# Performance work log

Measured on AMD Instinct MI355X. Metric: run time of the kernel, lower is better.

## Reference

```python
import jax, jax.numpy as jnp
import numpy as np

# config constants (init_kwargs)
S, C, N, DK, DA = 4, 1024, 131072, 128, 2048
M_TOP, K_MAX, B, T = 32, 64, 64, 1.0
EPS = 1e-8


def setup_inputs() -> dict:
    key = jax.random.key(0)
    k0, k1, k2, k3 = jax.random.split(key, 4)
    return {
        "z": jax.random.normal(k0, (B, DA), jnp.float32),
        "pool_keys": jax.random.normal(k1, (S, N, DK), jnp.float32),
        "W_Q": jax.random.normal(k2, (S, DK, DA), jnp.float32) * DA ** -0.5,
        "aspect_weights": jnp.zeros((S,), jnp.float32),
        "tau": jnp.zeros((), jnp.float32),
        "centroids": jax.random.normal(k3, (S, C, DK), jnp.float32) * DK ** -0.5,
        "lambda_val": jnp.ones((), jnp.float32),
        "is_warmup": 0,
    }


def _l2norm(x):
    return x / (jnp.linalg.norm(x, axis=-1, keepdims=True) + EPS)


def reference(z, pool_keys, W_Q, aspect_weights, tau, centroids, lambda_val, is_warmup):
    Bb = z.shape[0]
    # aspect queries: [B, S, d_k]
    queries = jnp.einsum('ska,ba->bsk', W_Q, z)
    q_norm = _l2norm(queries)
    w = jax.nn.softmax(aspect_weights, axis=0)  # [S]

    # --- IVF stage 1: centroid search ---
    c_norm = _l2norm(centroids)                     # [S, C, d_k]
    c_sim = jnp.einsum('bsk,sck->bsc', q_norm, c_norm)
    c_score = jnp.einsum('s,bsc->bc', w, c_sim)      # [B, C]
    m_eff = min(M_TOP, C)
    _, top_clusters = jax.lax.top_k(c_score, m_eff)  # [B, m]

    # --- IVF stage 2: refine within selected clusters ---
    n_per_c = N // C
    cand_idx = (top_clusters[:, :, None] * n_per_c
                + jnp.arange(n_per_c)[None, None, :]).reshape(Bb, m_eff * n_per_c)  # [B, M]
    # gather candidate keys: [S, B, M, d_k] -> [B, S, M, d_k]
    keys_refine = jnp.take(pool_keys, cand_idx, axis=1).transpose(1, 0, 2, 3)
    k_norm = _l2norm(keys_refine)
    sim_ref = jnp.einsum('bsk,bsnk->bsn', q_norm, k_norm)
    s_i = jnp.einsum('s,bsn->bn', w, sim_ref)        # [B, M]

    # --- redundant full dense pass for soft_full ---
    p_norm_full = _l2norm(pool_keys)                 # [S, N, d_k]
    sim_all = jnp.einsum('bsk,snk->bsn', q_norm, p_norm_full)
    s_i_full = jnp.einsum('s,bsn->bn', w, sim_all)   # [B, N]
    soft_full = jax.nn.softmax(s_i_full / T, axis=-1)

    if is_warmup:
        scores, local_idx = jax.lax.top_k(s_i, K_MAX)
        global_idx = jnp.take_along_axis(cand_idx, local_idx, axis=1)
        alphas = jax.nn.softmax(scores / T, axis=-1)
    else:
        g = jax.nn.sigmoid(lambda_val * (s_i - tau))
        raw = g * jnp.exp(s_i / T)
        raw = raw / (raw.sum(axis=-1, keepdims=True) + EPS)
        top_raw, local_idx = jax.lax.top_k(raw, K_MAX)
        global_idx = jnp.take_along_axis(cand_idx, local_idx, axis=1)
        alphas = top_raw / (top_raw.sum(axis=-1, keepdims=True) + EPS)
    return alphas, global_idx, soft_full
```

## Files before the change

### kernel.cpp

```cpp
#include <hip/hip_runtime.h>
#include <math.h>

#define S_N   4
#define C_N   1024
#define N_N   131072
#define DK_N  128
#define DA_N  2048
#define MTOP  32
#define KMAX  64
#define B_N   64
#define NPC   128
#define MCAND 4096
#define KTOT  512
#define EPSF  1e-8f

__global__ void k_init(float* sums) { sums[threadIdx.x] = 0.0f; }

__global__ __launch_bounds__(256) void k_queries(const float* __restrict__ z,
                                                 const float* __restrict__ wqm,
                                                 const float* __restrict__ aw,
                                                 float* __restrict__ qw) {
    __shared__ __align__(16) float zl[DA_N];
    __shared__ float ql[DK_N];
    __shared__ float red[2];
    const int t = threadIdx.x;
    const int s = blockIdx.x >> 6;
    const int b = blockIdx.x & 63;
    const float4* zr = (const float4*)(z + (size_t)b * DA_N);
    float4* zl4 = (float4*)zl;
    for (int i = t; i < DA_N / 4; i += 256) zl4[i] = zr[i];
    __syncthreads();
    const int wave = t >> 6, lane = t & 63;
    for (int kw = 0; kw < 32; ++kw) {
        int k = wave * 32 + kw;
        const float* wr = wqm + ((size_t)(s * DK_N + k)) * DA_N;
        float acc = 0.f;
        #pragma unroll
        for (int i = 0; i < 32; ++i) acc += wr[i * 64 + lane] * zl[i * 64 + lane];
        for (int m = 32; m >= 1; m >>= 1) acc += __shfl_xor(acc, m, 64);
        if (lane == 0) ql[k] = acc;
    }
    __syncthreads();
    if (t < 128) {
        float v = ql[t];
        float p = v * v;
        for (int m = 32; m >= 1; m >>= 1) p += __shfl_xor(p, m, 64);
        if ((t & 63) == 0) red[t >> 6] = p;
    }
    __syncthreads();
    if (t < 128) {
        float ss = red[0] + red[1];
        float inv = 1.0f / (sqrtf(ss) + EPSF);
        float a0 = aw[0], a1 = aw[1], a2 = aw[2], a3 = aw[3];
        float mx = fmaxf(fmaxf(a0, a1), fmaxf(a2, a3));
        float e0 = expf(a0 - mx), e1 = expf(a1 - mx), e2 = expf(a2 - mx), e3 = expf(a3 - mx);
        float wsum = e0 + e1 + e2 + e3;
        float wv = (s == 0 ? e0 : s == 1 ? e1 : s == 2 ? e2 : e3) / wsum;
        qw[(size_t)b * KTOT + s * DK_N + t] = wv * inv * ql[t];
    }
}

__global__ __launch_bounds__(256) void k_cnorm(const float* __restrict__ cent,
                                               float* __restrict__ cn) {
    const int t = threadIdx.x;
    const int wave = t >> 6, lane = t & 63;
    const int row = blockIdx.x * 4 + wave;
    const float2* cr = (const float2*)(cent + (size_t)row * DK_N);
    float2 v = cr[lane];
    float p = v.x * v.x + v.y * v.y;
    for (int m = 32; m >= 1; m >>= 1) p += __shfl_xor(p, m, 64);
    float inv = 1.0f / (sqrtf(p) + EPSF);
    float2* o = (float2*)(cn + (size_t)row * DK_N);
    o[lane] = make_float2(v.x * inv, v.y * inv);
}

__global__ __launch_bounds__(256) void k_cscore(const float* __restrict__ qw,
                                                const float* __restrict__ cn,
                                                double* __restrict__ cs) {
    __shared__ __align__(16) float qwl[KTOT];
    const int t = threadIdx.x;
    const int b = blockIdx.x >> 2;
    const int cq = blockIdx.x & 3;
    qwl[t] = qw[(size_t)b * KTOT + t];
    qwl[t + 256] = qw[(size_t)b * KTOT + t + 256];
    __syncthreads();
    const int c = cq * 256 + t;
    double acc = 0.0;
    #pragma unroll
    for (int s = 0; s < 4; ++s) {
        const float* qs = qwl + s * DK_N;
        const float4* cp = (const float4*)(cn + ((size_t)(s * C_N + c)) * DK_N);
        #pragma unroll 8
        for (int k4 = 0; k4 < 32; ++k4) {
            float4 f = cp[k4];
            acc += (double)qs[k4 * 4 + 0] * f.x + (double)qs[k4 * 4 + 1] * f.y
                 + (double)qs[k4 * 4 + 2] * f.z + (double)qs[k4 * 4 + 3] * f.w;
        }
    }
    cs[(size_t)b * C_N + c] = acc;
}

__global__ __launch_bounds__(256) void k_top32(const double* __restrict__ cs,
                                               int* __restrict__ topc,
                                               int* __restrict__ invm) {
    __shared__ double val[C_N];
    __shared__ double wvs[4];
    __shared__ int wis[4];
    const int t = threadIdx.x;
    const int b = blockIdx.x;
    #pragma unroll
    for (int r = 0; r < 4; ++r) {
        val[r * 256 + t] = cs[(size_t)b * C_N + r * 256 + t];
        invm[b * C_N + r * 256 + t] = -1;
    }
    __syncthreads();
    for (int it = 0; it < MTOP; ++it) {
        double bv = -1e300; int bi = -1;
        #pragma unroll
        for (int r = 0; r < 4; ++r) {
            int cc = r * 256 + t;
            double v = val[cc];
            if (v > bv || (v == bv && (unsigned)cc < (unsigned)bi)) { bv = v; bi = cc; }
        }
        for (int m = 32; m >= 1; m >>= 1) {
            double ov = __shfl_xor(bv, m, 64);
            int oi = __shfl_xor(bi, m, 64);
            if (ov > bv || (ov == bv && (unsigned)oi < (unsigned)bi)) { bv = ov; bi = oi; }
        }
        if ((t & 63) == 0) { wvs[t >> 6] = bv; wis[t >> 6] = bi; }
        __syncthreads();
        if (t == 0) {
            double cbv = wvs[0]; int cbi = wis[0];
            for (int w = 1; w < 4; ++w)
                if (wvs[w] > cbv || (wvs[w] == cbv && (unsigned)wis[w] < (unsigned)cbi)) { cbv = wvs[w]; cbi = wis[w]; }
            topc[b * MTOP + it] = cbi;
            invm[b * C_N + cbi] = it;
            val[cbi] = -1e300;
        }
        __syncthreads();
    }
}

__global__ __launch_bounds__(256, 4) void k_dense(const float* __restrict__ keys,
                                                  const float* __restrict__ qw,
                                                  const int* __restrict__ invm,
                                                  double* __restrict__ si,
                                                  float* __restrict__ out_soft,
                                                  float* __restrict__ sums) {
    __shared__ __align__(16) float keyl[32 * 196];
    __shared__ __align__(16) float qwl[32 * 68];
    __shared__ float invn[128];
    __shared__ int hb[64], hj[64];
    __shared__ int hcnt;
    const int t = threadIdx.x;
    const int cl = blockIdx.x;
    const int n0 = cl * NPC;
    if (t == 0) hcnt = 0;
    __syncthreads();
    if (t < 64) {
        int j = invm[t * C_N + cl];
        if (j >= 0) { int p = atomicAdd(&hcnt, 1); hb[p] = t; hj[p] = j; }
    }
    const int nq = t & 15, bq = t >> 4;
    float acc[4][8];
    #pragma unroll
    for (int i = 0; i < 4; ++i)
        #pragma unroll
        for (int j = 0; j < 8; ++j) acc[i][j] = 0.f;

    for (int c = 0; c < 16; ++c) {
        const int s = c >> 2;
        const int koff = (c & 3) * 32;
        if ((c & 3) == 0) {
            __syncthreads();
            int row = t >> 1, half = t & 1;
            const float4* kp4 = (const float4*)(keys + ((size_t)(s * N_N + n0 + row)) * DK_N + half * 64);
            float ssq = 0.f;
            #pragma unroll
            for (int i = 0; i < 16; ++i) {
                float4 f = kp4[i];
                ssq += f.x * f.x + f.y * f.y + f.z * f.z + f.w * f.w;
            }
            ssq += __shfl_xor(ssq, 1, 64);
            if (half == 0) invn[row] = 1.0f / (sqrtf(ssq) + EPSF);
            __syncthreads();
        }
        #pragma unroll
        for (int rep = 0; rep < 4; ++rep) {
            int idx = rep * 256 + t;
            int kk4 = idx & 7;
            int n = idx >> 3;
            const float4 v = *(const float4*)(keys + ((size_t)(s * N_N + n0 + n)) * DK_N + koff + kk4 * 4);
            float sc = invn[n];
            int noffn = n + ((n >> 3) << 2);
            float vv[4] = {v.x * sc, v.y * sc, v.z * sc, v.w * sc};
            #pragma unroll
            for (int jj = 0; jj < 4; ++jj) {
                int j2 = (kk4 + jj) & 3;
                keyl[(kk4 * 4 + j2) * 196 + noffn] = vv[j2];
            }
        }
        #pragma unroll
        for (int rep = 0; rep < 2; ++rep) {
            int idx = rep * 256 + t;
            int kk4 = idx & 7;
            int b = idx >> 3;
            const float4 v = *(const float4*)(qw + (size_t)b * KTOT + c * 32 + kk4 * 4);
            float vv[4] = {v.x, v.y, v.z, v.w};
            #pragma unroll
            for (int jj = 0; jj < 4; ++jj) {
                int j2 = (kk4 + jj) & 3;
                qwl[(kk4 * 4 + j2) * 68 + b] = vv[j2];
            }
        }
        __syncthreads();
        #pragma unroll 4
        for (int k = 0; k < 32; ++k) {
            const float4 qv = *(const float4*)&qwl[k * 68 + bq * 4];
            const float4 ka = *(const float4*)&keyl[k * 196 + nq * 12];
            const float4 kb = *(const float4*)&keyl[k * 196 + nq * 12 + 4];
            const float qr[4] = {qv.x, qv.y, qv.z, qv.w};
            const float kr[8] = {ka.x, ka.y, ka.z, ka.w, kb.x, kb.y, kb.z, kb.w};
            #pragma unroll
            for (int i = 0; i < 4; ++i)
                #pragma unroll
                for (int j = 0; j < 8; ++j)
                    acc[i][j] += qr[i] * kr[j];
        }
        const int nh = hcnt;
        for (int h = 0; h < nh; ++h) {
            const int b = hb[h], j = hj[h];
            const int n = t >> 1, half = t & 1;
            const int noffn = n + ((n >> 3) << 2);
            double a = 0.0;
            #pragma unroll
            for (int kk2 = 0; kk2 < 16; ++kk2) {
                int kk = half * 16 + kk2;
                a += (double)qwl[kk * 68 + b] * (double)keyl[kk * 196 + noffn];
            }
            a += __shfl_xor(a, 1, 64);
            if (half == 0) {
                double* sp = si + (size_t)b * MCAND + j * NPC + n;
                if (c == 0) *sp = a;
                else *sp += a;
            }
        }
        __syncthreads();
    }
    #pragma unroll
    for (int i = 0; i < 4; ++i) {
        int b = bq * 4 + i;
        float e[8]; float se = 0.f;
        #pragma unroll
        for (int j = 0; j < 8; ++j) { e[j] = expf(acc[i][j]); se += e[j]; }
        float4* op = (float4*)(out_soft + (size_t)b * N_N + n0 + nq * 8);
        op[0] = make_float4(e[0], e[1], e[2], e[3]);
        op[1] = make_float4(e[4], e[5], e[6], e[7]);
        #pragma unroll
        for (int m = 8; m >= 1; m >>= 1) se += __shfl_xor(se, m, 16);
        if ((t & 15) == 0) atomicAdd(&sums[b], se);
    }
}

__global__ __launch_bounds__(256) void k_top64(const double* __restrict__ si,
                                               const int* __restrict__ topc,
                                               const float* __restrict__ taup,
                                               const float* __restrict__ lamp,
                                               const int* __restrict__ warmp,
                                               float* __restrict__ out_alpha,
                                               float* __restrict__ out_idx) {
    __shared__ double key64[MCAND];
    __shared__ float aux[MCAND];
    __shared__ double rs[4];
    __shared__ double wvs[4];
    __shared__ int wis[4];
    __shared__ int sel[KMAX];
    const int t = threadIdx.x;
    const int b = blockIdx.x;
    const int warm = *warmp;
    const float lamf = *lamp, tauf = *taup;
    double loc = 0.0;
    for (int r = 0; r < 16; ++r) {
        int j = r * 256 + t;
        double sd = si[(size_t)b * MCAND + j];
        float sf = (float)sd;
        if (warm) {
            key64[j] = sd;
            aux[j] = sf;
        } else {
            float g = 1.0f / (1.0f + expf(-lamf * (sf - tauf)));
            float raw = g * expf(sf);
            aux[j] = raw;
            loc += (double)raw;
            double x = (double)lamf * (sd - (double)tauf);
            key64[j] = sd - log1p(exp(-x));
        }
    }
    for (int m = 32; m >= 1; m >>= 1) loc += __shfl_xor(loc, m, 64);
    if ((t & 63) == 0) rs[t >> 6] = loc;
    __syncthreads();
    const float S_all = (float)(rs[0] + rs[1] + rs[2] + rs[3]);
    for (int it = 0; it < KMAX; ++it) {
        double bv = -1e300; int bi = -1;
        for (int r = 0; r < 16; ++r) {
            int j = r * 256 + t;
            double v = key64[j];
            if (v > bv || (v == bv && (unsigned)j < (unsigned)bi)) { bv = v; bi = j; }
        }
        for (int m = 32; m >= 1; m >>= 1) {
            double ov = __shfl_xor(bv, m, 64);
            int oi = __shfl_xor(bi, m, 64);
            if (ov > bv || (ov == bv && (unsigned)oi < (unsigned)bi)) { bv = ov; bi = oi; }
        }
        if ((t & 63) == 0) { wvs[t >> 6] = bv; wis[t >> 6] = bi; }
        __syncthreads();
        if (t == 0) {
            double cbv = wvs[0]; int cbi = wis[0];
            for (int w = 1; w < 4; ++w)
                if (wvs[w] > cbv || (wvs[w] == cbv && (unsigned)wis[w] < (unsigned)cbi)) { cbv = wvs[w]; cbi = wis[w]; }
            sel[it] = cbi;
            key64[cbi] = -1e300;
        }
        __syncthreads();
    }
    if (t < KMAX) {
        int j = sel[t];
        float numer;
        if (warm) numer = expf(aux[j]);
        else numer = aux[j] / (S_all + EPSF);
        float tot = numer;
        for (int m = 32; m >= 1; m >>= 1) tot += __shfl_xor(tot, m, 64);
        float denom = warm ? tot : (tot + EPSF);
        float alpha = numer / denom;
        out_alpha[b * KMAX + t] = alpha;
        int cl2 = topc[b * MTOP + (j >> 7)];
        out_idx[b * KMAX + t] = (float)(cl2 * NPC + (j & 127));
    }
}

__global__ void k_norm(float* __restrict__ out_soft, const float* __restrict__ sums) {
    const int b = blockIdx.x >> 7;
    const int p = (blockIdx.x & 127) * 256 + threadIdx.x;
    const float inv = 1.0f / sums[b];
    float4* p4 = (float4*)(out_soft + (size_t)b * N_N) + p;
    float4 v = *p4;
    v.x *= inv; v.y *= inv; v.z *= inv; v.w *= inv;
    *p4 = v;
}

extern "C" void kernel_launch(void* const* d_in, const int* in_sizes, int n_in,
                              void* d_out, int out_size, void* d_ws, size_t ws_size,
                              hipStream_t stream) {
    const float* z    = (const float*)d_in[0];
    const float* keys = (const float*)d_in[1];
    const float* wqm  = (const float*)d_in[2];
    const float* aw   = (const float*)d_in[3];
    const float* tau  = (const float*)d_in[4];
    const float* cent = (const float*)d_in[5];
    const float* lam  = (const float*)d_in[6];
    const int*   warm = (const int*)d_in[7];
    float* out = (float*)d_out;
    float* out_alpha = out;
    float* out_idx   = out + B_N * KMAX;
    float* out_soft  = out + 2 * B_N * KMAX;
    char* ws = (char*)d_ws;
    float*  qw   = (float*)(ws + 0);
    float*  cn   = (float*)(ws + 131072);
    double* cs   = (double*)(ws + 2228224);
    int*    topc = (int*)(ws + 2752512);
    int*    invm = (int*)(ws + 2760704);
    double* si   = (double*)(ws + 3022848);
    float*  sums = (float*)(ws + 5120000);

    hipLaunchKernelGGL(k_init,    dim3(1),    dim3(64),  0, stream, sums);
    hipLaunchKernelGGL(k_queries, dim3(256),  dim3(256), 0, stream, z, wqm, aw, qw);
    hipLaunchKernelGGL(k_cnorm,   dim3(1024), dim3(256), 0, stream, cent, cn);
    hipLaunchKernelGGL(k_cscore,  dim3(256),  dim3(256), 0, stream, qw, cn, cs);
    hipLaunchKernelGGL(k_top32,   dim3(64),   dim3(256), 0, stream, cs, topc, invm);
    hipLaunchKernelGGL(k_dense,   dim3(1024), dim3(256), 0, stream, keys, qw, invm, si, out_soft, sums);
    hipLaunchKernelGGL(k_top64,   dim3(64),   dim3(256), 0, stream, si, topc, tau, lam, warm, out_alpha, out_idx);
    hipLaunchKernelGGL(k_norm,    dim3(8192), dim3(256), 0, stream, out_soft, sums);
}
```

Before: 758.4 us.

## Use bf16 MFMA for dense similarity, parallelize top-64 and centroid scoring

Result: faster. 688.0 us (-9.3%).

```diff
diff --git a/kernel.cpp b/kernel.cpp
--- a/kernel.cpp
+++ b/kernel.cpp
@@ -13,6 +13,15 @@
 #define MCAND 4096
 #define KTOT  512
 #define EPSF  1e-8f
+#define KPAD  40
+
+typedef short s8v __attribute__((ext_vector_type(8)));
+typedef float f4v __attribute__((ext_vector_type(4)));
+
+__device__ __forceinline__ unsigned short f2bf(float x) {
+    unsigned u = __float_as_uint(x);
+    return (unsigned short)((u + 0x7FFFu + ((u >> 16) & 1u)) >> 16);
+}
 
 __global__ void k_init(float* sums) { sums[threadIdx.x] = 0.0f; }
 
@@ -78,26 +87,27 @@
                                                 const float* __restrict__ cn,
                                                 double* __restrict__ cs) {
     __shared__ __align__(16) float qwl[KTOT];
-    const int t = threadIdx.x;
-    const int b = blockIdx.x >> 2;
-    const int cq = blockIdx.x & 3;
+    __shared__ double part[4][64];
+    const int t = threadIdx.x;
+    const int b = blockIdx.x >> 4;
+    const int cq = blockIdx.x & 15;
     qwl[t] = qw[(size_t)b * KTOT + t];
     qwl[t + 256] = qw[(size_t)b * KTOT + t + 256];
     __syncthreads();
-    const int c = cq * 256 + t;
+    const int cl = t & 63, s = t >> 6;
+    const int c = cq * 64 + cl;
+    const float* qs = qwl + s * DK_N;
+    const float4* cp = (const float4*)(cn + ((size_t)(s * C_N + c)) * DK_N);
     double acc = 0.0;
-    #pragma unroll
-    for (int s = 0; s < 4; ++s) {
-        const float* qs = qwl + s * DK_N;
-        const float4* cp = (const float4*)(cn + ((size_t)(s * C_N + c)) * DK_N);
-        #pragma unroll 8
-        for (int k4 = 0; k4 < 32; ++k4) {
-            float4 f = cp[k4];
-            acc += (double)qs[k4 * 4 + 0] * f.x + (double)qs[k4 * 4 + 1] * f.y
-                 + (double)qs[k4 * 4 + 2] * f.z + (double)qs[k4 * 4 + 3] * f.w;
-        }
-    }
-    cs[(size_t)b * C_N + c] = acc;
+    #pragma unroll 8
+    for (int k4 = 0; k4 < 32; ++k4) {
+        float4 f = cp[k4];
+        acc += (double)qs[k4 * 4 + 0] * f.x + (double)qs[k4 * 4 + 1] * f.y
+             + (double)qs[k4 * 4 + 2] * f.z + (double)qs[k4 * 4 + 3] * f.w;
+    }
+    part[s][cl] = acc;
+    __syncthreads();
+    if (t < 64) cs[(size_t)b * C_N + cq * 64 + t] = part[0][t] + part[1][t] + part[2][t] + part[3][t];
 }
 
 __global__ __launch_bounds__(256) void k_top32(const double* __restrict__ cs,
@@ -147,26 +157,29 @@
                                                   double* __restrict__ si,
                                                   float* __restrict__ out_soft,
                                                   float* __restrict__ sums) {
-    __shared__ __align__(16) float keyl[32 * 196];
-    __shared__ __align__(16) float qwl[32 * 68];
+    __shared__ __align__(16) unsigned short keyl[128 * KPAD];
+    __shared__ __align__(16) unsigned short qbl[64 * KPAD];
+    __shared__ float qf32l[32 * 68];
     __shared__ float invn[128];
+    __shared__ double hacc[8 * 128];
     __shared__ int hb[64], hj[64];
     __shared__ int hcnt;
     const int t = threadIdx.x;
     const int cl = blockIdx.x;
     const int n0 = cl * NPC;
+    const int lane = t & 63, w = t >> 6;
+    const int quad = lane >> 4, col = lane & 15;
     if (t == 0) hcnt = 0;
+    for (int i = t; i < 1024; i += 256) hacc[i] = 0.0;
     __syncthreads();
     if (t < 64) {
         int j = invm[t * C_N + cl];
         if (j >= 0) { int p = atomicAdd(&hcnt, 1); hb[p] = t; hj[p] = j; }
     }
-    const int nq = t & 15, bq = t >> 4;
-    float acc[4][8];
+
+    f4v acc[8];
     #pragma unroll
-    for (int i = 0; i < 4; ++i)
-        #pragma unroll
-        for (int j = 0; j < 8; ++j) acc[i][j] = 0.f;
+    for (int T = 0; T < 8; ++T) acc[T] = (f4v){0.f, 0.f, 0.f, 0.f};
 
     for (int c = 0; c < 16; ++c) {
         const int s = c >> 2;
@@ -192,13 +205,9 @@
             int n = idx >> 3;
             const float4 v = *(const float4*)(keys + ((size_t)(s * N_N + n0 + n)) * DK_N + koff + kk4 * 4);
             float sc = invn[n];
-            int noffn = n + ((n >> 3) << 2);
-            float vv[4] = {v.x * sc, v.y * sc, v.z * sc, v.w * sc};
-            #pragma unroll
-            for (int jj = 0; jj < 4; ++jj) {
-                int j2 = (kk4 + jj) & 3;
-                keyl[(kk4 * 4 + j2) * 196 + noffn] = vv[j2];
-            }
+            unsigned w0 = (unsigned)f2bf(v.x * sc) | ((unsigned)f2bf(v.y * sc) << 16);
+            unsigned w1 = (unsigned)f2bf(v.z * sc) | ((unsigned)f2bf(v.w * sc) << 16);
+            *(uint2*)&keyl[n * KPAD + kk4 * 4] = make_uint2(w0, w1);
         }
         #pragma unroll
         for (int rep = 0; rep < 2; ++rep) {
@@ -206,59 +215,68 @@
             int kk4 = idx & 7;
             int b = idx >> 3;
             const float4 v = *(const float4*)(qw + (size_t)b * KTOT + c * 32 + kk4 * 4);
-            float vv[4] = {v.x, v.y, v.z, v.w};
-            #pragma unroll
-            for (int jj = 0; jj < 4; ++jj) {
-                int j2 = (kk4 + jj) & 3;
-                qwl[(kk4 * 4 + j2) * 68 + b] = vv[j2];
-            }
+            unsigned w0 = (unsigned)f2bf(v.x) | ((unsigned)f2bf(v.y) << 16);
+            unsigned w1 = (unsigned)f2bf(v.z) | ((unsigned)f2bf(v.w) << 16);
+            *(uint2*)&qbl[b * KPAD + kk4 * 4] = make_uint2(w0, w1);
+            qf32l[(kk4 * 4 + 0) * 68 + b] = v.x;
+            qf32l[(kk4 * 4 + 1) * 68 + b] = v.y;
+            qf32l[(kk4 * 4 + 2) * 68 + b] = v.z;
+            qf32l[(kk4 * 4 + 3) * 68 + b] = v.w;
         }
         __syncthreads();
-        #pragma unroll 4
-        for (int k = 0; k < 32; ++k) {
-            const float4 qv = *(const float4*)&qwl[k * 68 + bq * 4];
-            const float4 ka = *(const float4*)&keyl[k * 196 + nq * 12];
-            const float4 kb = *(const float4*)&keyl[k * 196 + nq * 12 + 4];
-            const float qr[4] = {qv.x, qv.y, qv.z, qv.w};
-            const float kr[8] = {ka.x, ka.y, ka.z, ka.w, kb.x, kb.y, kb.z, kb.w};
-            #pragma unroll
-            for (int i = 0; i < 4; ++i)
-                #pragma unroll
-                for (int j = 0; j < 8; ++j)
-                    acc[i][j] += qr[i] * kr[j];
+        const s8v a_frag = *(const s8v*)&qbl[(w * 16 + col) * KPAD + quad * 8];
+        #pragma unroll
+        for (int T = 0; T < 8; ++T) {
+            const s8v b_frag = *(const s8v*)&keyl[(T * 16 + col) * KPAD + quad * 8];
+            acc[T] = __builtin_amdgcn_mfma_f32_16x16x32_bf16(a_frag, b_frag, acc[T], 0, 0, 0);
         }
         const int nh = hcnt;
         for (int h = 0; h < nh; ++h) {
             const int b = hb[h], j = hj[h];
             const int n = t >> 1, half = t & 1;
-            const int noffn = n + ((n >> 3) << 2);
+            const float4* kp = (const float4*)(keys + ((size_t)(s * N_N + n0 + n)) * DK_N + koff + half * 16);
             double a = 0.0;
             #pragma unroll
-            for (int kk2 = 0; kk2 < 16; ++kk2) {
-                int kk = half * 16 + kk2;
-                a += (double)qwl[kk * 68 + b] * (double)keyl[kk * 196 + noffn];
+            for (int e = 0; e < 4; ++e) {
+                float4 kv = kp[e];
+                int kb = half * 16 + e * 4;
+                a += (double)qf32l[(kb + 0) * 68 + b] * kv.x
+                   + (double)qf32l[(kb + 1) * 68 + b] * kv.y
+                   + (double)qf32l[(kb + 2) * 68 + b] * kv.z
+                   + (double)qf32l[(kb + 3) * 68 + b] * kv.w;
             }
             a += __shfl_xor(a, 1, 64);
             if (half == 0) {
-                double* sp = si + (size_t)b * MCAND + j * NPC + n;
-                if (c == 0) *sp = a;
-                else *sp += a;
+                a *= (double)invn[n];
+                if (h < 8) hacc[h * 128 + n] += a;
+                else {
+                    double* sp = si + (size_t)b * MCAND + j * NPC + n;
+                    if (c == 0) *sp = a;
+                    else *sp += a;
+                }
             }
         }
         __syncthreads();
     }
+    {
+        const int nh = hcnt < 8 ? hcnt : 8;
+        if (t < 128)
+            for (int h = 0; h < nh; ++h)
+                si[(size_t)hb[h] * MCAND + hj[h] * NPC + t] = hacc[h * 128 + t];
+    }
     #pragma unroll
-    for (int i = 0; i < 4; ++i) {
-        int b = bq * 4 + i;
-        float e[8]; float se = 0.f;
-        #pragma unroll
-        for (int j = 0; j < 8; ++j) { e[j] = expf(acc[i][j]); se += e[j]; }
-        float4* op = (float4*)(out_soft + (size_t)b * N_N + n0 + nq * 8);
-        op[0] = make_float4(e[0], e[1], e[2], e[3]);
-        op[1] = make_float4(e[4], e[5], e[6], e[7]);
-        #pragma unroll
-        for (int m = 8; m >= 1; m >>= 1) se += __shfl_xor(se, m, 16);
-        if ((t & 15) == 0) atomicAdd(&sums[b], se);
+    for (int r = 0; r < 4; ++r) {
+        const int b = w * 16 + quad * 4 + r;
+        float se = 0.f;
+        #pragma unroll
+        for (int T = 0; T < 8; ++T) {
+            float ev = expf(acc[T][r]);
+            out_soft[(size_t)b * N_N + n0 + T * 16 + col] = ev;
+            se += ev;
+        }
+        #pragma unroll
+        for (int m = 8; m >= 1; m >>= 1) se += __shfl_xor(se, m, 64);
+        if (col == 0) atomicAdd(&sums[b], se);
     }
 }
 
@@ -269,60 +287,87 @@
                                                const int* __restrict__ warmp,
                                                float* __restrict__ out_alpha,
                                                float* __restrict__ out_idx) {
-    __shared__ double key64[MCAND];
     __shared__ float aux[MCAND];
+    __shared__ double selk[256];
+    __shared__ int selj[256];
     __shared__ double rs[4];
-    __shared__ double wvs[4];
-    __shared__ int wis[4];
     __shared__ int sel[KMAX];
     const int t = threadIdx.x;
     const int b = blockIdx.x;
+    const int w = t >> 6, lane = t & 63;
     const int warm = *warmp;
     const float lamf = *lamp, tauf = *taup;
+    double v[16];
     double loc = 0.0;
+    #pragma unroll
     for (int r = 0; r < 16; ++r) {
-        int j = r * 256 + t;
+        int j = w * 1024 + r * 64 + lane;
         double sd = si[(size_t)b * MCAND + j];
         float sf = (float)sd;
+        double key;
         if (warm) {
-            key64[j] = sd;
             aux[j] = sf;
+            key = sd;
         } else {
             float g = 1.0f / (1.0f + expf(-lamf * (sf - tauf)));
             float raw = g * expf(sf);
             aux[j] = raw;
             loc += (double)raw;
-            double x = (double)lamf * (sd - (double)tauf);
-            key64[j] = sd - log1p(exp(-x));
-        }
+            if (lamf >= 0.0f) key = sd;
+            else {
+                double x = (double)lamf * (sd - (double)tauf);
+                key = sd - log1p(exp(-x));
+            }
+        }
+        v[r] = key;
     }
     for (int m = 32; m >= 1; m >>= 1) loc += __shfl_xor(loc, m, 64);
-    if ((t & 63) == 0) rs[t >> 6] = loc;
+    if (lane == 0) rs[w] = loc;
+    double bv = -1e300; int br = -1;
+    #pragma unroll
+    for (int r = 0; r < 16; ++r)
+        if (v[r] > bv) { bv = v[r]; br = r; }
+    for (int round = 0; round < KMAX; ++round) {
+        double cv = bv;
+        int cj = (br >= 0) ? (w * 1024 + br * 64 + lane) : 0x7FFFFFFF;
+        #pragma unroll
+        for (int m = 32; m >= 1; m >>= 1) {
+            double ov = __shfl_xor(cv, m, 64);
+            int oj = __shfl_xor(cj, m, 64);
+            if (ov > cv || (ov == cv && oj < cj)) { cv = ov; cj = oj; }
+        }
+        if (lane == 0) { selk[w * 64 + round] = cv; selj[w * 64 + round] = cj; }
+        if (cj == w * 1024 + br * 64 + lane) {
+            v[br] = -1e300;
+            bv = -1e300; br = -1;
+            #pragma unroll
+            for (int r = 0; r < 16; ++r)
+                if (v[r] > bv) { bv = v[r]; br = r; }
+        }
+    }
+    __syncthreads();
+    if (w == 0) {
+        double fv[4]; int fj[4];
+        #pragma unroll
+        for (int i = 0; i < 4; ++i) { fv[i] = selk[lane * 4 + i]; fj[i] = selj[lane * 4 + i]; }
+        for (int round = 0; round < KMAX; ++round) {
+            double cv = -1e300; int cj = 0x7FFFFFFF; int ci = -1;
+            #pragma unroll
+            for (int i = 0; i < 4; ++i)
+                if (fv[i] > cv || (fv[i] == cv && fj[i] < cj)) { cv = fv[i]; cj = fj[i]; ci = i; }
+            double wv2 = cv; int wj = cj;
+            #pragma unroll
+            for (int m = 32; m >= 1; m >>= 1) {
+                double ov = __shfl_xor(wv2, m, 64);
+                int oj = __shfl_xor(wj, m, 64);
+                if (ov > wv2 || (ov == wv2 && oj < wj)) { wv2 = ov; wj = oj; }
+            }
+            if (wj == cj && ci >= 0) fv[ci] = -1e300;
+            if (lane == 0) sel[round] = wj;
+        }
+    }
     __syncthreads();
     const float S_all = (float)(rs[0] + rs[1] + rs[2] + rs[3]);
-    for (int it = 0; it < KMAX; ++it) {
-        double bv = -1e300; int bi = -1;
-        for (int r = 0; r < 16; ++r) {
-            int j = r * 256 + t;
-            double v = key64[j];
-            if (v > bv || (v == bv && (unsigned)j < (unsigned)bi)) { bv = v; bi = j; }
-        }
-        for (int m = 32; m >= 1; m >>= 1) {
-            double ov = __shfl_xor(bv, m, 64);
-            int oi = __shfl_xor(bi, m, 64);
-            if (ov > bv || (ov == bv && (unsigned)oi < (unsigned)bi)) { bv = ov; bi = oi; }
-        }
-        if ((t & 63) == 0) { wvs[t >> 6] = bv; wis[t >> 6] = bi; }
-        __syncthreads();
-        if (t == 0) {
-            double cbv = wvs[0]; int cbi = wis[0];
-            for (int w = 1; w < 4; ++w)
-                if (wvs[w] > cbv || (wvs[w] == cbv && (unsigned)wis[w] < (unsigned)cbi)) { cbv = wvs[w]; cbi = wis[w]; }
-            sel[it] = cbi;
-            key64[cbi] = -1e300;
-        }
-        __syncthreads();
-    }
     if (t < KMAX) {
         int j = sel[t];
         float numer;
@@ -375,7 +420,7 @@
     hipLaunchKernelGGL(k_init,    dim3(1),    dim3(64),  0, stream, sums);
     hipLaunchKernelGGL(k_queries, dim3(256),  dim3(256), 0, stream, z, wqm, aw, qw);
     hipLaunchKernelGGL(k_cnorm,   dim3(1024), dim3(256), 0, stream, cent, cn);
-    hipLaunchKernelGGL(k_cscore,  dim3(256),  dim3(256), 0, stream, qw, cn, cs);
+    hipLaunchKernelGGL(k_cscore,  dim3(1024), dim3(256), 0, stream, qw, cn, cs);
     hipLaunchKernelGGL(k_top32,   dim3(64),   dim3(256), 0, stream, cs, topc, invm);
     hipLaunchKernelGGL(k_dense,   dim3(1024), dim3(256), 0, stream, keys, qw, invm, si, out_soft, sums);
     hipLaunchKernelGGL(k_top64,   dim3(64),   dim3(256), 0, stream, si, topc, tau, lam, warm, out_alpha, out_idx);
```
